# Kernel tuning notes

Hardware: AMD Instinct MI355X
Metric: run time of the kernel (lower is better)

The kernel has to match this reference:

```python
import jax, jax.numpy as jnp
import numpy as np

N_NODES = 50000
N_EDGES = 800000
X_DIM, H_DIM, Y_DIM = 128, 256, 128


def spmm(adj_vals, adj_row, adj_col, x):
    # sparse [N,N] @ dense [N,D] via gather + segment scatter-add
    msgs = adj_vals[:, None] * x[adj_col]  # [E, D]
    return jax.ops.segment_sum(msgs, adj_row, num_segments=N_NODES)


def setup_inputs() -> dict:
    key = jax.random.key(0)
    ks = jax.random.split(key, 6)
    x = jax.random.uniform(ks[0], (N_NODES, X_DIM), dtype=jnp.float32)
    adj_vals = jax.random.uniform(ks[1], (N_EDGES,), dtype=jnp.float32)
    adj_row = jax.random.randint(ks[2], (N_EDGES,), 0, N_NODES, dtype=jnp.int32)
    adj_col = jax.random.randint(ks[3], (N_EDGES,), 0, N_NODES, dtype=jnp.int32)
    W1 = jax.random.normal(ks[4], (X_DIM, H_DIM), dtype=jnp.float32) * (1.0 / np.sqrt(X_DIM))
    b1 = jnp.zeros((H_DIM,), dtype=jnp.float32)
    W2 = jax.random.normal(ks[5], (H_DIM, Y_DIM), dtype=jnp.float32) * (1.0 / np.sqrt(H_DIM))
    b2 = jnp.zeros((Y_DIM,), dtype=jnp.float32)
    return {"x": x, "adj_vals": adj_vals, "adj_row": adj_row, "adj_col": adj_col,
            "W1": W1, "b1": b1, "W2": W2, "b2": b2}


def reference(x, adj_vals, adj_row, adj_col, W1, b1, W2, b2):
    # row-normalize features: x / (sum_j x_ij + 1e-4)
    x = x / (jnp.sum(x, axis=1, keepdims=True) + 1e-4)
    # layer 1: spmm -> linear -> relu (dropout is identity at eval)
    h = jax.nn.relu(spmm(adj_vals, adj_row, adj_col, x) @ W1 + b1)  # [N, H]
    # layer 2: spmm -> linear
    y = spmm(adj_vals, adj_row, adj_col, h) @ W2 + b2  # [N, Y]
    return y
```

## Files before the change

### kernel.cpp

```cpp
#include <hip/hip_runtime.h>

#define N_NODES 50000
#define N_EDGES 800000
#define X_DIM 128
#define H_DIM 256
#define Y_DIM 128

typedef unsigned int uint32;
typedef unsigned short ushort16;
typedef __attribute__((ext_vector_type(8))) short short8;
typedef __attribute__((ext_vector_type(4))) float floatx4;

__device__ inline ushort16 f2bf(float f) {
    uint32 u = __float_as_uint(f);
    return (ushort16)((u + 0x7FFFu + ((u >> 16) & 1u)) >> 16);
}
__device__ inline float bf_lo(uint32 u) { return __uint_as_float(u << 16); }
__device__ inline float bf_hi(uint32 u) { return __uint_as_float(u & 0xFFFF0000u); }

__device__ inline float ub0(uint32 u) { return (float)(u & 0xFFu); }
__device__ inline float ub1(uint32 u) { return (float)((u >> 8) & 0xFFu); }
__device__ inline float ub2(uint32 u) { return (float)((u >> 16) & 0xFFu); }
__device__ inline float ub3(uint32 u) { return (float)(u >> 24); }

#define BUCKET_SHIFT 7
#define NB 391
#define CHUNK 4096
#define NCHUNK 196
#define CAP_B 2560

#define NORM_BLOCKS 12500
#define CONV_BLOCKS 256

__global__ __launch_bounds__(256) void prep_kernel(
    const float* __restrict__ x, unsigned short* __restrict__ xq,
    float* __restrict__ scales,
    const float* __restrict__ W1, const float* __restrict__ W2,
    ushort16* __restrict__ W1t, ushort16* __restrict__ W2t,
    const int* __restrict__ rows, int* __restrict__ gpartial) {
    int b = blockIdx.x;
    if (b < NORM_BLOCKS) {
        int row = (b * 256 + threadIdx.x) >> 6;
        int lane = threadIdx.x & 63;
        float2 v = ((const float2*)x)[(size_t)row * 64 + lane];
        float s = v.x + v.y;
        float m = fmaxf(v.x, v.y);
        #pragma unroll
        for (int off = 32; off > 0; off >>= 1) {
            s += __shfl_xor(s, off, 64);
            m = fmaxf(m, __shfl_xor(m, off, 64));
        }
        float inv = 1.0f / (s + 1e-4f);
        float rq = (m > 0.f) ? 127.f / m : 0.f;
        int q0 = (int)(v.x * rq + 0.5f);
        int q1 = (int)(v.y * rq + 0.5f);
        xq[(size_t)row * 64 + lane] = (unsigned short)(q0 | (q1 << 8));
        if (lane == 0) scales[row] = m * inv * (1.f / 127.f);
    } else if (b < NORM_BLOCKS + CONV_BLOCKS) {
        int t = (b - NORM_BLOCKS) * 256 + threadIdx.x;
        if (t < X_DIM * H_DIM) {
            int n = t >> 7, k = t & 127;
            W1t[t] = f2bf(W1[k * H_DIM + n]);
        } else {
            int u = t - X_DIM * H_DIM;
            int y = u >> 8, k = u & 255;
            W2t[u] = f2bf(W2[k * Y_DIM + y]);
        }
    } else {
        __shared__ int h[NB];
        int j = b - NORM_BLOCKS - CONV_BLOCKS;
        int t = threadIdx.x;
        for (int i = t; i < NB; i += 256) h[i] = 0;
        __syncthreads();
        int base = j * CHUNK;
        #pragma unroll
        for (int k = 0; k < CHUNK / 256; k++) {
            int e = base + t + k * 256;
            if (e < N_EDGES) atomicAdd(&h[rows[e] >> BUCKET_SHIFT], 1);
        }
        __syncthreads();
        for (int i = t; i < NB; i += 256) gpartial[j * NB + i] = h[i];
    }
}

__global__ __launch_bounds__(512) void bucket_scan_kernel(
    const int* __restrict__ gpartial, int* __restrict__ bucket_base,
    int* __restrict__ bcursor, int* __restrict__ rowptr) {
    __shared__ int s[512];
    int t = threadIdx.x;
    int total = 0;
    if (t < NB) {
        #pragma unroll 4
        for (int j = 0; j < NCHUNK; j++) total += gpartial[j * NB + t];
    }
    s[t] = total;
    __syncthreads();
    #pragma unroll
    for (int off = 1; off < 512; off <<= 1) {
        int u = (t >= off) ? s[t - off] : 0;
        __syncthreads();
        s[t] += u;
        __syncthreads();
    }
    if (t < NB) {
        int excl = s[t] - total;
        bucket_base[t] = excl;
        bcursor[t] = excl;
    }
    if (t == 0) { bucket_base[NB] = N_EDGES; rowptr[N_NODES] = N_EDGES; }
}

__global__ __launch_bounds__(512) void bucketize_kernel(
    const int* __restrict__ rows, const int* __restrict__ cols,
    const float* __restrict__ vals, const int* __restrict__ gpartial,
    int* __restrict__ bcursor, int2* __restrict__ edges) {
    __shared__ int ob[512];
    __shared__ int c[NB];
    __shared__ int g[NB];
    __shared__ int2 buf[CHUNK];
    int t = threadIdx.x;
    int j = blockIdx.x;
    int base = j * CHUNK;
    int M = N_EDGES - base; if (M > CHUNK) M = CHUNK;
    int cnt = (t < NB) ? gpartial[j * NB + t] : 0;
    ob[t] = cnt;
    __syncthreads();
    #pragma unroll
    for (int off = 1; off < 512; off <<= 1) {
        int u = (t >= off) ? ob[t - off] : 0;
        __syncthreads();
        ob[t] += u;
        __syncthreads();
    }
    ob[t] -= cnt;
    if (t < NB) {
        c[t] = 0;
        g[t] = (cnt > 0) ? atomicAdd(&bcursor[t], cnt) : 0;
    }
    __syncthreads();
    #pragma unroll
    for (int k = 0; k < CHUNK / 512; k++) {
        int e = base + t + k * 512;
        if (e < N_EDGES) {
            int r = rows[e];
            int bb = r >> BUCKET_SHIFT;
            int p = ob[bb] + atomicAdd(&c[bb], 1);
            buf[p] = make_int2(cols[e] | ((r & 127) << 16) | (bb << 23),
                               __float_as_int(vals[e]));
        }
    }
    __syncthreads();
    for (int i = t; i < M; i += 512) {
        int2 e = buf[i];
        int bb = (int)((uint32)e.x >> 23);
        edges[g[bb] + (i - ob[bb])] = e;
    }
}

__global__ __launch_bounds__(256) void bucket_sort_kernel(
    const int* __restrict__ bucket_base, int2* __restrict__ edges,
    int2* __restrict__ scratch, int* __restrict__ rowptr) {
    __shared__ int2 buf[CAP_B];
    __shared__ int2 buf2[CAP_B];
    __shared__ int h[128], o[128], c[128];
    int b = blockIdx.x, t = threadIdx.x;
    int base = bucket_base[b];
    int cnt = bucket_base[b + 1] - base;
    bool fits = (cnt <= CAP_B);
    if (t < 128) h[t] = 0;
    __syncthreads();
    for (int i = t; i < cnt; i += 256) {
        int2 e = edges[base + i];
        if (fits) buf[i] = e; else scratch[base + i] = e;
        atomicAdd(&h[(e.x >> 16) & 127], 1);
    }
    __syncthreads();
    int valh = (t < 128) ? h[t] : 0;
    #pragma unroll
    for (int off = 1; off < 128; off <<= 1) {
        int u = (t >= off && t < 128) ? h[t - off] : 0;
        __syncthreads();
        if (t < 128) h[t] += u;
        __syncthreads();
    }
    if (t < 128) {
        o[t] = h[t] - valh;
        c[t] = 0;
        int i = (b << BUCKET_SHIFT) + t;
        if (i < N_NODES) rowptr[i] = base + h[t] - valh;
    }
    __syncthreads();
    for (int i = t; i < cnt; i += 256) {
        int2 e = fits ? buf[i] : scratch[base + i];
        int lr = (e.x >> 16) & 127;
        int p = o[lr] + atomicAdd(&c[lr], 1);
        if (fits) buf2[p] = e; else edges[base + p] = e;
    }
    __syncthreads();
    if (fits)
        for (int i = t; i < cnt; i += 256) edges[base + i] = buf2[i];
}

__device__ __forceinline__ void spmm_row4_q8(const uint2* __restrict__ xq2,
                                             const float* __restrict__ scales,
                                             const int2* __restrict__ edges,
                                             int start, int end, int lane,
                                             float A[8]) {
    const int g16 = lane & 15;
    const int bsrc = lane & 48;
    int cur = start;
    while (__any(cur < end)) {
        int n = end - cur;
        n = n < 0 ? 0 : (n > 16 ? 16 : n);
        int2 ev = make_int2(0, 0);
        float sc = 0.f;
        if (g16 < n) {
            ev = edges[cur + g16];
            sc = scales[ev.x & 0xFFFF];
        }
        int c = ev.x & 0xFFFF;
        float vs = __int_as_float(ev.y) * sc;
        int n0 = __shfl(n, 0, 64), n1 = __shfl(n, 16, 64);
        int n2 = __shfl(n, 32, 64), n3 = __shfl(n, 48, 64);
        int nm = max(max(n0, n1), max(n2, n3));
        int jm = (nm + 7) & ~7;
        for (int j = 0; j < jm; j += 8) {
            uint2 f[8];
            float vv[8];
            #pragma unroll
            for (int u = 0; u < 8; u++) {
                int cc = __shfl(c, bsrc + j + u, 64);
                vv[u] = __shfl(vs, bsrc + j + u, 64);
                f[u] = xq2[(size_t)cc * 16 + g16];
            }
            #pragma unroll
            for (int u = 0; u < 8; u++) {
                A[0] += vv[u] * ub0(f[u].x); A[1] += vv[u] * ub1(f[u].x);
                A[2] += vv[u] * ub2(f[u].x); A[3] += vv[u] * ub3(f[u].x);
                A[4] += vv[u] * ub0(f[u].y); A[5] += vv[u] * ub1(f[u].y);
                A[6] += vv[u] * ub2(f[u].y); A[7] += vv[u] * ub3(f[u].y);
            }
        }
        cur += n;
    }
}

__device__ __forceinline__ void spmm_row4(const uint4* __restrict__ feat4,
                                          const int2* __restrict__ edges,
                                          int start, int end, int lane,
                                          float A[8]) {
    const int g16 = lane & 15;
    const int bsrc = lane & 48;
    int cur = start;
    while (__any(cur < end)) {
        int n = end - cur;
        n = n < 0 ? 0 : (n > 16 ? 16 : n);
        int2 ev = make_int2(0, 0);
        if (g16 < n) ev = edges[cur + g16];
        int c = ev.x & 0xFFFF;
        float v = __int_as_float(ev.y);
        int n0 = __shfl(n, 0, 64), n1 = __shfl(n, 16, 64);
        int n2 = __shfl(n, 32, 64), n3 = __shfl(n, 48, 64);
        int nm = max(max(n0, n1), max(n2, n3));
        int jm = (nm + 7) & ~7;
        for (int j = 0; j < jm; j += 8) {
            uint4 f[8];
            float vv[8];
            #pragma unroll
            for (int u = 0; u < 8; u++) {
                int cc = __shfl(c, bsrc + j + u, 64);
                vv[u] = __shfl(v, bsrc + j + u, 64);
                f[u] = feat4[(size_t)cc * 16 + g16];
            }
            #pragma unroll
            for (int u = 0; u < 8; u++) {
                A[0] += vv[u] * bf_lo(f[u].x); A[1] += vv[u] * bf_hi(f[u].x);
                A[2] += vv[u] * bf_lo(f[u].y); A[3] += vv[u] * bf_hi(f[u].y);
                A[4] += vv[u] * bf_lo(f[u].z); A[5] += vv[u] * bf_hi(f[u].z);
                A[6] += vv[u] * bf_lo(f[u].w); A[7] += vv[u] * bf_hi(f[u].w);
            }
        }
        cur += n;
    }
}

__global__ __launch_bounds__(512, 4) void spmm_gemm_fused(
    const uint32* __restrict__ xq, const float* __restrict__ scales,
    const int* __restrict__ rowptr,
    const int2* __restrict__ edges, const ushort16* __restrict__ W1t,
    const ushort16* __restrict__ W2t, const float* __restrict__ b1,
    ushort16* __restrict__ hw) {
    __shared__ ushort16 a_s[64 * 136];
    __shared__ ushort16 h_s[64 * 264];
    const int tx = threadIdx.x;
    const int wave = tx >> 6, lane = tx & 63;
    const int quad = lane >> 4, l16 = lane & 15;
    const int row0 = blockIdx.x * 64;

    for (int i = 0; i < 2; i++) {
        int r = wave * 8 + i * 4 + quad;
        int row = row0 + r;
        int s = 0, e = 0;
        if (row < N_NODES) { s = rowptr[row]; e = rowptr[row + 1]; }
        float A[8] = {0.f, 0.f, 0.f, 0.f, 0.f, 0.f, 0.f, 0.f};
        spmm_row4_q8((const uint2*)xq, scales, edges, s, e, lane, A);
        uint4 pk;
        pk.x = (uint32)f2bf(A[0]) | ((uint32)f2bf(A[1]) << 16);
        pk.y = (uint32)f2bf(A[2]) | ((uint32)f2bf(A[3]) << 16);
        pk.z = (uint32)f2bf(A[4]) | ((uint32)f2bf(A[5]) << 16);
        pk.w = (uint32)f2bf(A[6]) | ((uint32)f2bf(A[7]) << 16);
        *(uint4*)&a_s[r * 136 + l16 * 8] = pk;
    }

    short8 bfr1[2][4];
    #pragma unroll
    for (int ct = 0; ct < 2; ct++)
        #pragma unroll
        for (int kk = 0; kk < 4; kk++)
            bfr1[ct][kk] = *(const short8*)
                &W1t[(wave * 32 + ct * 16 + l16) * 128 + kk * 32 + quad * 8];
    __syncthreads();

    floatx4 acc1[4][2];
    #pragma unroll
    for (int rs = 0; rs < 4; rs++)
        #pragma unroll
        for (int ct = 0; ct < 2; ct++)
            #pragma unroll
            for (int j = 0; j < 4; j++) acc1[rs][ct][j] = 0.f;
    #pragma unroll
    for (int kk = 0; kk < 4; kk++) {
        #pragma unroll
        for (int rs = 0; rs < 4; rs++) {
            short8 af = *(const short8*)&a_s[(rs * 16 + l16) * 136 + kk * 32 + quad * 8];
            #pragma unroll
            for (int ct = 0; ct < 2; ct++)
                acc1[rs][ct] = __builtin_amdgcn_mfma_f32_16x16x32_bf16(
                    af, bfr1[ct][kk], acc1[rs][ct], 0, 0, 0);
        }
    }
    float bv[2];
    #pragma unroll
    for (int ct = 0; ct < 2; ct++) bv[ct] = b1[wave * 32 + ct * 16 + l16];
    #pragma unroll
    for (int rs = 0; rs < 4; rs++)
        #pragma unroll
        for (int ct = 0; ct < 2; ct++)
            #pragma unroll
            for (int reg = 0; reg < 4; reg++) {
                float v = acc1[rs][ct][reg] + bv[ct];
                v = v > 0.f ? v : 0.f;
                h_s[(rs * 16 + quad * 4 + reg) * 264 + wave * 32 + ct * 16 + l16] = f2bf(v);
            }

    short8 bfr2[8];
    #pragma unroll
    for (int kk = 0; kk < 8; kk++)
        bfr2[kk] = *(const short8*)
            &W2t[(wave * 16 + l16) * 256 + kk * 32 + quad * 8];
    __syncthreads();

    floatx4 acc2[4];
    #pragma unroll
    for (int rs = 0; rs < 4; rs++)
        #pragma unroll
        for (int j = 0; j < 4; j++) acc2[rs][j] = 0.f;
    #pragma unroll
    for (int kk = 0; kk < 8; kk++) {
        #pragma unroll
        for (int rs = 0; rs < 4; rs++) {
            short8 af = *(const short8*)&h_s[(rs * 16 + l16) * 264 + kk * 32 + quad * 8];
            acc2[rs] = __builtin_amdgcn_mfma_f32_16x16x32_bf16(
                af, bfr2[kk], acc2[rs], 0, 0, 0);
        }
    }
    #pragma unroll
    for (int rs = 0; rs < 4; rs++)
        #pragma unroll
        for (int reg = 0; reg < 4; reg++) {
            int row = row0 + rs * 16 + quad * 4 + reg;
            if (row < N_NODES)
                hw[(size_t)row * 128 + wave * 16 + l16] = f2bf(acc2[rs][reg]);
        }
}

__global__ __launch_bounds__(256, 4) void spmm_out_kernel(
    const uint32* __restrict__ feat, const int* __restrict__ rowptr,
    const int2* __restrict__ edges, const float* __restrict__ bias,
    float* __restrict__ out) {
    int w = (blockIdx.x * blockDim.x + threadIdx.x) >> 6;
    int lane = threadIdx.x & 63;
    int quad = lane >> 4, g16 = lane & 15;
    int row = w * 4 + quad;
    int s = rowptr[row], e = rowptr[row + 1];
    float A[8] = {0.f, 0.f, 0.f, 0.f, 0.f, 0.f, 0.f, 0.f};
    spmm_row4((const uint4*)feat, edges, s, e, lane, A);
    float4 b0 = ((const float4*)bias)[g16 * 2];
    float4 b1 = ((const float4*)bias)[g16 * 2 + 1];
    ((float4*)out)[(size_t)row * 32 + g16 * 2] =
        make_float4(A[0] + b0.x, A[1] + b0.y, A[2] + b0.z, A[3] + b0.w);
    ((float4*)out)[(size_t)row * 32 + g16 * 2 + 1] =
        make_float4(A[4] + b1.x, A[5] + b1.y, A[6] + b1.z, A[7] + b1.w);
}

extern "C" void kernel_launch(void* const* d_in, const int* in_sizes, int n_in,
                              void* d_out, int out_size, void* d_ws, size_t ws_size,
                              hipStream_t stream) {
    const float* x = (const float*)d_in[0];
    const float* adj_vals = (const float*)d_in[1];
    const int* adj_row = (const int*)d_in[2];
    const int* adj_col = (const int*)d_in[3];
    const float* W1 = (const float*)d_in[4];
    const float* b1 = (const float*)d_in[5];
    const float* W2 = (const float*)d_in[6];
    const float* b2 = (const float*)d_in[7];
    float* out = (float*)d_out;

    char* ws = (char*)d_ws;
    unsigned short* xq = (unsigned short*)(ws + 0);
    float*    scales   = (float*)   (ws + 6400000);
    ushort16* hw       = (ushort16*)(ws + 6600000);
    int2*     edges    = (int2*)    (ws + 19400000);
    int2*     scratch  = (int2*)    (ws + 25800000);
    int*      gpartial = (int*)     (ws + 32200000);
    int*      rowptr   = (int*)     (ws + 32507008);
    int*      bbase    = (int*)     (ws + 32708000);
    int*      bcursor  = (int*)     (ws + 32710048);
    ushort16* W1t      = (ushort16*)(ws + 32712096);
    ushort16* W2t      = (ushort16*)(ws + 32777632);

    hipLaunchKernelGGL(prep_kernel, dim3(NORM_BLOCKS + CONV_BLOCKS + NCHUNK),
                       dim3(256), 0, stream, x, xq, scales, W1, W2, W1t, W2t,
                       adj_row, gpartial);

    hipLaunchKernelGGL(bucket_scan_kernel, dim3(1), dim3(512),
                       0, stream, gpartial, bbase, bcursor, rowptr);

    hipLaunchKernelGGL(bucketize_kernel, dim3(NCHUNK), dim3(512),
                       0, stream, adj_row, adj_col, adj_vals, gpartial, bcursor, edges);
    hipLaunchKernelGGL(bucket_sort_kernel, dim3(NB), dim3(256),
                       0, stream, bbase, edges, scratch, rowptr);

    hipLaunchKernelGGL(spmm_gemm_fused, dim3((N_NODES + 63) / 64), dim3(512),
                       0, stream, (const uint32*)xq, scales, rowptr, edges,
                       W1t, W2t, b1, hw);

    hipLaunchKernelGGL(spmm_out_kernel, dim3(N_NODES / 16), dim3(256),
                       0, stream, (const uint32*)hw, rowptr, edges, b2, out);
}
```

Before: 216.2 us.

## Split fused GEMM stage into two row halves to raise occupancy

The fused SpMM+two-GEMM kernel now processes its 64-row tile in two 32-row halves for the GEMM stages. This halves the h_s shared buffer and the accumulator registers, and the launch bounds ask for 8 blocks per CU instead of 4, so more waves can hide the latency of the irregular gather. In exchange it adds an extra barrier per half, reloads the W1/W2 fragments twice, and risks register spills under the tighter bound.

```diff
diff --git a/kernel.cpp b/kernel.cpp
--- a/kernel.cpp
+++ b/kernel.cpp
@@ -284,14 +284,14 @@
     }
 }
 
-__global__ __launch_bounds__(512, 4) void spmm_gemm_fused(
+__global__ __launch_bounds__(512, 8) void spmm_gemm_fused(
     const uint32* __restrict__ xq, const float* __restrict__ scales,
     const int* __restrict__ rowptr,
     const int2* __restrict__ edges, const ushort16* __restrict__ W1t,
     const ushort16* __restrict__ W2t, const float* __restrict__ b1,
     ushort16* __restrict__ hw) {
     __shared__ ushort16 a_s[64 * 136];
-    __shared__ ushort16 h_s[64 * 264];
+    __shared__ ushort16 h_s[32 * 264];
     const int tx = threadIdx.x;
     const int wave = tx >> 6, lane = tx & 63;
     const int quad = lane >> 4, l16 = lane & 15;
@@ -311,77 +311,85 @@
         pk.w = (uint32)f2bf(A[6]) | ((uint32)f2bf(A[7]) << 16);
         *(uint4*)&a_s[r * 136 + l16 * 8] = pk;
     }
-
-    short8 bfr1[2][4];
-    #pragma unroll
-    for (int ct = 0; ct < 2; ct++)
-        #pragma unroll
-        for (int kk = 0; kk < 4; kk++)
-            bfr1[ct][kk] = *(const short8*)
-                &W1t[(wave * 32 + ct * 16 + l16) * 128 + kk * 32 + quad * 8];
-    __syncthreads();
-
-    floatx4 acc1[4][2];
-    #pragma unroll
-    for (int rs = 0; rs < 4; rs++)
+    __syncthreads();
+
+    float bv[2];
+    #pragma unroll
+    for (int ct = 0; ct < 2; ct++) bv[ct] = b1[wave * 32 + ct * 16 + l16];
+
+    #pragma unroll
+    for (int hf = 0; hf < 2; hf++) {
+        if (hf) __syncthreads();
+
+        short8 bfr1[2][4];
         #pragma unroll
         for (int ct = 0; ct < 2; ct++)
             #pragma unroll
-            for (int j = 0; j < 4; j++) acc1[rs][ct][j] = 0.f;
-    #pragma unroll
-    for (int kk = 0; kk < 4; kk++) {
-        #pragma unroll
-        for (int rs = 0; rs < 4; rs++) {
-            short8 af = *(const short8*)&a_s[(rs * 16 + l16) * 136 + kk * 32 + quad * 8];
+            for (int kk = 0; kk < 4; kk++)
+                bfr1[ct][kk] = *(const short8*)
+                    &W1t[(wave * 32 + ct * 16 + l16) * 128 + kk * 32 + quad * 8];
+        floatx4 acc1[2][2];
+        #pragma unroll
+        for (int rs2 = 0; rs2 < 2; rs2++)
             #pragma unroll
             for (int ct = 0; ct < 2; ct++)
-                acc1[rs][ct] = __builtin_amdgcn_mfma_f32_16x16x32_bf16(
-                    af, bfr1[ct][kk], acc1[rs][ct], 0, 0, 0);
-        }
-    }
-    float bv[2];
-    #pragma unroll
-    for (int ct = 0; ct < 2; ct++) bv[ct] = b1[wave * 32 + ct * 16 + l16];
-    #pragma unroll
-    for (int rs = 0; rs < 4; rs++)
-        #pragma unroll
-        for (int ct = 0; ct < 2; ct++)
+                #pragma unroll
+                for (int j = 0; j < 4; j++) acc1[rs2][ct][j] = 0.f;
+        #pragma unroll
+        for (int kk = 0; kk < 4; kk++) {
+            #pragma unroll
+            for (int rs2 = 0; rs2 < 2; rs2++) {
+                short8 af = *(const short8*)
+                    &a_s[((hf * 2 + rs2) * 16 + l16) * 136 + kk * 32 + quad * 8];
+                #pragma unroll
+                for (int ct = 0; ct < 2; ct++)
+                    acc1[rs2][ct] = __builtin_amdgcn_mfma_f32_16x16x32_bf16(
+                        af, bfr1[ct][kk], acc1[rs2][ct], 0, 0, 0);
+            }
+        }
+        #pragma unroll
+        for (int rs2 = 0; rs2 < 2; rs2++)
+            #pragma unroll
+            for (int ct = 0; ct < 2; ct++)
+                #pragma unroll
+                for (int reg = 0; reg < 4; reg++) {
+                    float v = acc1[rs2][ct][reg] + bv[ct];
+                    v = v > 0.f ? v : 0.f;
+                    h_s[(rs2 * 16 + quad * 4 + reg) * 264 + wave * 32 + ct * 16 + l16]
+                        = f2bf(v);
+                }
+
+        short8 bfr2[8];
+        #pragma unroll
+        for (int kk = 0; kk < 8; kk++)
+            bfr2[kk] = *(const short8*)
+                &W2t[(wave * 16 + l16) * 256 + kk * 32 + quad * 8];
+        __syncthreads();
+
+        floatx4 acc2[2];
+        #pragma unroll
+        for (int rs2 = 0; rs2 < 2; rs2++)
+            #pragma unroll
+            for (int j = 0; j < 4; j++) acc2[rs2][j] = 0.f;
+        #pragma unroll
+        for (int kk = 0; kk < 8; kk++) {
+            #pragma unroll
+            for (int rs2 = 0; rs2 < 2; rs2++) {
+                short8 af = *(const short8*)
+                    &h_s[(rs2 * 16 + l16) * 264 + kk * 32 + quad * 8];
+                acc2[rs2] = __builtin_amdgcn_mfma_f32_16x16x32_bf16(
+                    af, bfr2[kk], acc2[rs2], 0, 0, 0);
+            }
+        }
+        #pragma unroll
+        for (int rs2 = 0; rs2 < 2; rs2++)
             #pragma unroll
             for (int reg = 0; reg < 4; reg++) {
-                float v = acc1[rs][ct][reg] + bv[ct];
-                v = v > 0.f ? v : 0.f;
-                h_s[(rs * 16 + quad * 4 + reg) * 264 + wave * 32 + ct * 16 + l16] = f2bf(v);
-            }
-
-    short8 bfr2[8];
-    #pragma unroll
-    for (int kk = 0; kk < 8; kk++)
-        bfr2[kk] = *(const short8*)
-            &W2t[(wave * 16 + l16) * 256 + kk * 32 + quad * 8];
-    __syncthreads();
-
-    floatx4 acc2[4];
-    #pragma unroll
-    for (int rs = 0; rs < 4; rs++)
-        #pragma unroll
-        for (int j = 0; j < 4; j++) acc2[rs][j] = 0.f;
-    #pragma unroll
-    for (int kk = 0; kk < 8; kk++) {
-        #pragma unroll
-        for (int rs = 0; rs < 4; rs++) {
-            short8 af = *(const short8*)&h_s[(rs * 16 + l16) * 264 + kk * 32 + quad * 8];
-            acc2[rs] = __builtin_amdgcn_mfma_f32_16x16x32_bf16(
-                af, bfr2[kk], acc2[rs], 0, 0, 0);
-        }
-    }
-    #pragma unroll
-    for (int rs = 0; rs < 4; rs++)
-        #pragma unroll
-        for (int reg = 0; reg < 4; reg++) {
-            int row = row0 + rs * 16 + quad * 4 + reg;
-            if (row < N_NODES)
-                hw[(size_t)row * 128 + wave * 16 + l16] = f2bf(acc2[rs][reg]);
-        }
+                int row = row0 + hf * 32 + rs2 * 16 + quad * 4 + reg;
+                if (row < N_NODES)
+                    hw[(size_t)row * 128 + wave * 16 + l16] = f2bf(acc2[rs2][reg]);
+            }
+    }
 }
 
 __global__ __launch_bounds__(256, 4) void spmm_out_kernel(
```

After: 226.5 us. +4.8%, slower.
